# Optimization experiments

Hardware: AMD Instinct MI355X
Metric: run time of the kernel (lower is better)

## Reference

```python
import jax, jax.numpy as jnp
from jax import lax
import numpy as np

B = 32768      # batch
D = 256        # input = hidden = output dim
DEPTH = 9      # universal_depth


def setup_inputs() -> dict:
    key = jax.random.key(0)
    ks = jax.random.split(key, 16)
    s = 1.0 / np.sqrt(D)  # keep pre-activations sane
    r = lambda k, shp, sc=s: (jax.random.normal(k, shp, jnp.float32) * sc)
    return {
        "x": jax.random.normal(ks[0], (B, D), jnp.float32),
        "lin0_w": r(ks[1], (D, D)), "lin0_b": r(ks[2], (D,), 0.1),
        "lin1_w": r(ks[3], (D, D)), "lin1_b": r(ks[4], (D,), 0.1),
        "u1_w": jax.random.normal(ks[5], (DEPTH, D, D), jnp.float32),
        "u1_cw": r(ks[6], (D, D)), "u1_cb": r(ks[7], (D,), 0.1),
        "lin2_w": r(ks[8], (D, D)), "lin2_b": r(ks[9], (D,), 0.1),
        "u2_w": jax.random.normal(ks[10], (DEPTH, D, D), jnp.float32),
        "u2_cw": r(ks[11], (D, D)), "u2_cb": r(ks[12], (D,), 0.1),
        "lino_w": r(ks[13], (D, D)), "lino_b": r(ks[14], (D,), 0.1),
    }


def _universal_layer(x, uw, cw, cb):
    """UniversalNeuralLayer.forward, vectorized.

    The circulant 'gate' matrix implements, for state s of length n:
        s'[i] = cos*s[i] - sin*s[(i+1)%n] + sin*s[(i-1)%n]
    Applied 3 times per depth with angles uw[d, j, 0..2] (j = output unit).
    The result is independent of x and of the batch index.
    """
    n = x.shape[1]
    classical = x @ cw + cb                      # [B, n]
    # angle sequence per output j, in (depth, gate) order -> [3*DEPTH, n]
    angles = jnp.transpose(uw[:, :, :3], (0, 2, 1)).reshape(-1, n)
    init = jnp.full((n, n), 1.0 / np.sqrt(n), dtype=x.dtype)  # [n_j, n_state]

    def step(s, ang):
        c = jnp.cos(ang)[:, None]
        sn = jnp.sin(ang)[:, None]
        return c * s + sn * (jnp.roll(s, 1, axis=1) - jnp.roll(s, -1, axis=1)), None

    s, _ = lax.scan(step, init, angles)
    p = s[:, 0] ** 2                             # |state[0]|^2 per output j
    return jnp.tanh(classical + p[None, :])


def reference(x, lin0_w, lin0_b, lin1_w, lin1_b, u1_w, u1_cw, u1_cb,
              lin2_w, lin2_b, u2_w, u2_cw, u2_cb, lino_w, lino_b):
    h = jax.nn.relu(x @ lin0_w.T + lin0_b)
    h = jax.nn.relu(h @ lin1_w.T + lin1_b)
    h = _universal_layer(h, u1_w, u1_cw, u1_cb)
    h = jax.nn.relu(h @ lin2_w.T + lin2_b)
    h = _universal_layer(h, u2_w, u2_cw, u2_cb)
    return jax.nn.relu(h @ lino_w.T + lino_b)
```

## Files before the change

### kernel.cpp

```cpp
#include <hip/hip_runtime.h>
#include <math.h>

#define DD 256

typedef float  f32x4  __attribute__((ext_vector_type(4)));
typedef short  bf16x8 __attribute__((ext_vector_type(8)));

__device__ __forceinline__ unsigned short f2bf(float f) {
    unsigned int u = __float_as_uint(f);
    u = (u + 0x7fffu + ((u >> 16) & 1u)) >> 16;
    return (unsigned short)u;
}
__device__ __forceinline__ float bf2f(unsigned int h16) {
    return __uint_as_float(h16 << 16);
}

__global__ __launch_bounds__(256)
void universal_p_kernel(const float* __restrict__ u1_w,
                        const float* __restrict__ u2_w,
                        float* __restrict__ p_out ) {
    const int j = threadIdx.x;
    const float* uw = blockIdx.x ? u2_w : u1_w;
    float s = 0.0625f;
#pragma unroll
    for (int d = 0; d < 9; ++d)
#pragma unroll
        for (int g = 0; g < 3; ++g)
            s *= cosf(uw[d * DD * DD + j * DD + g]);
    p_out[blockIdx.x * DD + j] = s * s;
}

__global__ __launch_bounds__(256)
void prep_weights(const float* __restrict__ w0, const float* __restrict__ w1,
                  const float* __restrict__ cw1, const float* __restrict__ w2,
                  const float* __restrict__ cw2, const float* __restrict__ wo,
                  unsigned short* __restrict__ wall) {
    const int gid  = blockIdx.x * 256 + threadIdx.x;
    const int mat  = gid >> 13;
    const int rem  = gid & 8191;
    const int wb   = rem >> 11;
    const int rem2 = rem & 2047;
    const int k0   = rem2 >> 8;
    const int rem3 = rem2 & 255;
    const int nt   = rem3 >> 6;
    const int lane = rem3 & 63;
    const int n  = wb * 64 + nt * 16 + (lane & 15);
    const int kb = k0 * 32 + (lane >> 4) * 8;

    const float* src;
    bool tr = false;
    switch (mat) {
        case 0: src = w0; break;
        case 1: src = w1; break;
        case 2: src = cw1; tr = true; break;
        case 3: src = w2; break;
        case 4: src = cw2; tr = true; break;
        default: src = wo; break;
    }
    unsigned short tmp[8];
#pragma unroll
    for (int j = 0; j < 8; ++j) {
        const float v = tr ? src[(kb + j) * DD + n] : src[n * DD + kb + j];
        tmp[j] = f2bf(v);
    }
    *(uint4*)&wall[mat * 65536 + wb * 16384 + k0 * 2048 + nt * 512 + lane * 8] =
        *(const uint4*)tmp;
}

__device__ __forceinline__ int chunk_idx(int m, int kc) {
    return kc * 32 + (m ^ (kc & 7));
}

__device__ __forceinline__ float fast_tanh(float x) {
    const float e = __expf(2.0f * x);
    return 1.0f - 2.0f * __builtin_amdgcn_rcpf(1.0f + e);
}

template <int MODE>
__device__ __forceinline__ void layer_step(uint4* h, bf16x8 (&wr)[2][4],
                                           const unsigned short* __restrict__ W,
                                           const unsigned short* __restrict__ Wn,
                                           const float* __restrict__ bias,
                                           const float* __restrict__ pv) {
    const int tid  = threadIdx.x;
    const int wave = tid >> 6;
    const int lane = tid & 63;
    const int quad = lane >> 4;
    const int l15  = lane & 15;
    const unsigned short* Wb  = W  + wave * 16384 + lane * 8;
    const unsigned short* Wnb = Wn + wave * 16384 + lane * 8;

    f32x4 acc[4][2];
#pragma unroll
    for (int nt = 0; nt < 4; ++nt)
#pragma unroll
        for (int mt = 0; mt < 2; ++mt) acc[nt][mt] = (f32x4){0.f, 0.f, 0.f, 0.f};

    bf16x8 h_f[2][2];
#pragma unroll
    for (int mt = 0; mt < 2; ++mt)
        h_f[0][mt] = *(const bf16x8*)&h[chunk_idx(mt * 16 + l15, quad)];

#pragma unroll
    for (int k0 = 0; k0 < 8; ++k0) {
        const int cur = k0 & 1, nxt = cur ^ 1;
        {
            const unsigned short* ws = (k0 < 7) ? &Wb[(k0 + 1) * 2048] : Wnb;
#pragma unroll
            for (int nt = 0; nt < 4; ++nt)
                wr[nxt][nt] = *(const bf16x8*)&ws[nt * 512];
        }
        if (k0 < 7) {
            const int kc = (k0 + 1) * 4 + quad;
#pragma unroll
            for (int mt = 0; mt < 2; ++mt)
                h_f[nxt][mt] = *(const bf16x8*)&h[chunk_idx(mt * 16 + l15, kc)];
        }
#pragma unroll
        for (int nt = 0; nt < 4; ++nt)
#pragma unroll
            for (int mt = 0; mt < 2; ++mt)
                acc[nt][mt] = __builtin_amdgcn_mfma_f32_16x16x32_bf16(
                    wr[cur][nt], h_f[cur][mt], acc[nt][mt], 0, 0, 0);
    }

    __syncthreads();

    const int nb = wave * 64;
#pragma unroll
    for (int nt = 0; nt < 4; ++nt) {
        const int n0 = nb + nt * 16 + quad * 4;
        f32x4 add = *(const f32x4*)&bias[n0];
        if (MODE == 1) add += *(const f32x4*)&pv[n0];
        const int kc_o = n0 >> 3;
        const int half = quad & 1;
#pragma unroll
        for (int mt = 0; mt < 2; ++mt) {
            const f32x4 v = acc[nt][mt] + add;
            float t0, t1, t2, t3;
            if (MODE == 1) {
                t0 = fast_tanh(v.x); t1 = fast_tanh(v.y);
                t2 = fast_tanh(v.z); t3 = fast_tanh(v.w);
            } else {
                t0 = fmaxf(v.x, 0.f); t1 = fmaxf(v.y, 0.f);
                t2 = fmaxf(v.z, 0.f); t3 = fmaxf(v.w, 0.f);
            }
            uint2 u;
            u.x = (unsigned int)f2bf(t0) | ((unsigned int)f2bf(t1) << 16);
            u.y = (unsigned int)f2bf(t2) | ((unsigned int)f2bf(t3) << 16);
            *(uint2*)((char*)&h[chunk_idx(mt * 16 + l15, kc_o)] + half * 8) = u;
        }
    }
    __syncthreads();
}

__global__ __launch_bounds__(256, 2)
void unet_fused(const float* __restrict__ x,
                const unsigned short* __restrict__ wall,
                const float* __restrict__ b0, const float* __restrict__ b1,
                const float* __restrict__ cb1, const float* __restrict__ b2,
                const float* __restrict__ cb2, const float* __restrict__ bo,
                const float* __restrict__ pbuf,
                float* __restrict__ out) {
    __shared__ uint4 h[1024];
    const int m0 = blockIdx.x * 32;
    const int tid = threadIdx.x;
    const int wave = tid >> 6;
    const int lane = tid & 63;

    bf16x8 wr[2][4];
    {
        const unsigned short* ws = wall + wave * 16384 + lane * 8;
#pragma unroll
        for (int nt = 0; nt < 4; ++nt)
            wr[0][nt] = *(const bf16x8*)&ws[nt * 512];
    }

    const int c4 = tid & 63;
    const int rbase = (tid >> 6) * 8;
    const int kc_s = c4 >> 1;
    const int half_s = c4 & 1;
#pragma unroll
    for (int i = 0; i < 8; ++i) {
        const int row = rbase + i;
        const float4 v = *(const float4*)&x[(size_t)(m0 + row) * DD + c4 * 4];
        uint2 u;
        u.x = (unsigned int)f2bf(v.x) | ((unsigned int)f2bf(v.y) << 16);
        u.y = (unsigned int)f2bf(v.z) | ((unsigned int)f2bf(v.w) << 16);
        *(uint2*)((char*)&h[chunk_idx(row, kc_s)] + half_s * 8) = u;
    }
    __syncthreads();

    layer_step<0>(h, wr, wall + 0 * 65536, wall + 1 * 65536, b0, nullptr);
    layer_step<0>(h, wr, wall + 1 * 65536, wall + 2 * 65536, b1, nullptr);
    layer_step<1>(h, wr, wall + 2 * 65536, wall + 3 * 65536, cb1, pbuf);
    layer_step<0>(h, wr, wall + 3 * 65536, wall + 4 * 65536, b2, nullptr);
    layer_step<1>(h, wr, wall + 4 * 65536, wall + 5 * 65536, cb2, pbuf + 256);
    layer_step<0>(h, wr, wall + 5 * 65536, wall + 0 * 65536, bo, nullptr);

#pragma unroll
    for (int i = 0; i < 8; ++i) {
        const int row = rbase + i;
        const uint2 u = *(const uint2*)((char*)&h[chunk_idx(row, kc_s)] + half_s * 8);
        float4 v;
        v.x = bf2f(u.x & 0xffffu); v.y = bf2f(u.x >> 16);
        v.z = bf2f(u.y & 0xffffu); v.w = bf2f(u.y >> 16);
        *(float4*)&out[(size_t)(m0 + row) * DD + c4 * 4] = v;
    }
}

extern "C" void kernel_launch(void* const* d_in, const int* in_sizes, int n_in,
                              void* d_out, int out_size, void* d_ws, size_t ws_size,
                              hipStream_t stream) {
    const float* x      = (const float*)d_in[0];
    const float* lin0_w = (const float*)d_in[1];
    const float* lin0_b = (const float*)d_in[2];
    const float* lin1_w = (const float*)d_in[3];
    const float* lin1_b = (const float*)d_in[4];
    const float* u1_w   = (const float*)d_in[5];
    const float* u1_cw  = (const float*)d_in[6];
    const float* u1_cb  = (const float*)d_in[7];
    const float* lin2_w = (const float*)d_in[8];
    const float* lin2_b = (const float*)d_in[9];
    const float* u2_w   = (const float*)d_in[10];
    const float* u2_cw  = (const float*)d_in[11];
    const float* u2_cb  = (const float*)d_in[12];
    const float* lino_w = (const float*)d_in[13];
    const float* lino_b = (const float*)d_in[14];

    float* out = (float*)d_out;
    unsigned short* wall = (unsigned short*)d_ws;
    float* pbuf = (float*)((char*)d_ws + 6 * 65536 * 2);

    universal_p_kernel<<<dim3(2), dim3(256), 0, stream>>>(u1_w, u2_w, pbuf);
    prep_weights<<<dim3(192), dim3(256), 0, stream>>>(
        lin0_w, lin1_w, u1_cw, lin2_w, u2_cw, lino_w, wall);
    unet_fused<<<dim3(1024), dim3(256), 0, stream>>>(
        x, wall, lin0_b, lin1_b, u1_cb, lin2_b, u2_cb, lino_b, pbuf, out);
}
```

Before: 154.8 us.

## Double-buffer LDS activations, merge prep kernels, write final layer directly to global

Activations now ping-pong between two LDS buffers, so each layer needs only one barrier instead of two, using a lighter waitcnt-plus-barrier. The last layer writes fp32 ReLU results straight from the accumulators to global memory, which removes the bf16 round trip through LDS and also keeps the output in full precision. The two setup kernels are merged into one launch, and the occupancy hint rises to 4 blocks per CU. The cost is doubled LDS per block (32KB) and possible register pressure under the tighter launch bound.

```diff
diff --git a/kernel.cpp b/kernel.cpp
--- a/kernel.cpp
+++ b/kernel.cpp
@@ -16,25 +16,24 @@
 }
 
 __global__ __launch_bounds__(256)
-void universal_p_kernel(const float* __restrict__ u1_w,
-                        const float* __restrict__ u2_w,
-                        float* __restrict__ p_out ) {
-    const int j = threadIdx.x;
-    const float* uw = blockIdx.x ? u2_w : u1_w;
-    float s = 0.0625f;
-#pragma unroll
-    for (int d = 0; d < 9; ++d)
-#pragma unroll
-        for (int g = 0; g < 3; ++g)
-            s *= cosf(uw[d * DD * DD + j * DD + g]);
-    p_out[blockIdx.x * DD + j] = s * s;
-}
-
-__global__ __launch_bounds__(256)
-void prep_weights(const float* __restrict__ w0, const float* __restrict__ w1,
-                  const float* __restrict__ cw1, const float* __restrict__ w2,
-                  const float* __restrict__ cw2, const float* __restrict__ wo,
-                  unsigned short* __restrict__ wall) {
+void prep_all(const float* __restrict__ w0, const float* __restrict__ w1,
+              const float* __restrict__ cw1, const float* __restrict__ w2,
+              const float* __restrict__ cw2, const float* __restrict__ wo,
+              const float* __restrict__ u1_w, const float* __restrict__ u2_w,
+              unsigned short* __restrict__ wall, float* __restrict__ p_out) {
+    if (blockIdx.x >= 192) {
+        const int j = threadIdx.x;
+        const int which = blockIdx.x - 192;
+        const float* uw = which ? u2_w : u1_w;
+        float s = 0.0625f;
+#pragma unroll
+        for (int d = 0; d < 9; ++d)
+#pragma unroll
+            for (int g = 0; g < 3; ++g)
+                s *= cosf(uw[d * DD * DD + j * DD + g]);
+        p_out[which * DD + j] = s * s;
+        return;
+    }
     const int gid  = blockIdx.x * 256 + threadIdx.x;
     const int mat  = gid >> 13;
     const int rem  = gid & 8191;
@@ -76,19 +75,24 @@
     return 1.0f - 2.0f * __builtin_amdgcn_rcpf(1.0f + e);
 }
 
+__device__ __forceinline__ void lds_barrier() {
+    asm volatile("s_waitcnt lgkmcnt(0)" ::: "memory");
+    __builtin_amdgcn_s_barrier();
+}
+
 template <int MODE>
-__device__ __forceinline__ void layer_step(uint4* h, bf16x8 (&wr)[2][4],
-                                           const unsigned short* __restrict__ W,
-                                           const unsigned short* __restrict__ Wn,
+__device__ __forceinline__ void layer_step(const uint4* hr, uint4* hw,
+                                           bf16x8 (&wr)[2][4],
+                                           const unsigned short* __restrict__ Wb,
+                                           const unsigned short* __restrict__ Wnb,
                                            const float* __restrict__ bias,
-                                           const float* __restrict__ pv) {
+                                           const float* __restrict__ pv,
+                                           float* __restrict__ out, int m0) {
     const int tid  = threadIdx.x;
     const int wave = tid >> 6;
     const int lane = tid & 63;
     const int quad = lane >> 4;
     const int l15  = lane & 15;
-    const unsigned short* Wb  = W  + wave * 16384 + lane * 8;
-    const unsigned short* Wnb = Wn + wave * 16384 + lane * 8;
 
     f32x4 acc[4][2];
 #pragma unroll
@@ -99,7 +103,7 @@
     bf16x8 h_f[2][2];
 #pragma unroll
     for (int mt = 0; mt < 2; ++mt)
-        h_f[0][mt] = *(const bf16x8*)&h[chunk_idx(mt * 16 + l15, quad)];
+        h_f[0][mt] = *(const bf16x8*)&hr[chunk_idx(mt * 16 + l15, quad)];
 
 #pragma unroll
     for (int k0 = 0; k0 < 8; ++k0) {
@@ -114,7 +118,7 @@
             const int kc = (k0 + 1) * 4 + quad;
 #pragma unroll
             for (int mt = 0; mt < 2; ++mt)
-                h_f[nxt][mt] = *(const bf16x8*)&h[chunk_idx(mt * 16 + l15, kc)];
+                h_f[nxt][mt] = *(const bf16x8*)&hr[chunk_idx(mt * 16 + l15, kc)];
         }
 #pragma unroll
         for (int nt = 0; nt < 4; ++nt)
@@ -124,37 +128,48 @@
                     wr[cur][nt], h_f[cur][mt], acc[nt][mt], 0, 0, 0);
     }
 
-    __syncthreads();
-
     const int nb = wave * 64;
+    f32x4 addv[4];
 #pragma unroll
     for (int nt = 0; nt < 4; ++nt) {
         const int n0 = nb + nt * 16 + quad * 4;
-        f32x4 add = *(const f32x4*)&bias[n0];
-        if (MODE == 1) add += *(const f32x4*)&pv[n0];
+        addv[nt] = *(const f32x4*)&bias[n0];
+        if (MODE == 1) addv[nt] += *(const f32x4*)&pv[n0];
+    }
+
+#pragma unroll
+    for (int nt = 0; nt < 4; ++nt) {
+        const int n0   = nb + nt * 16 + quad * 4;
         const int kc_o = n0 >> 3;
         const int half = quad & 1;
 #pragma unroll
         for (int mt = 0; mt < 2; ++mt) {
-            const f32x4 v = acc[nt][mt] + add;
-            float t0, t1, t2, t3;
-            if (MODE == 1) {
-                t0 = fast_tanh(v.x); t1 = fast_tanh(v.y);
-                t2 = fast_tanh(v.z); t3 = fast_tanh(v.w);
+            const f32x4 v = acc[nt][mt] + addv[nt];
+            if (MODE == 2) {
+                f32x4 r;
+                r.x = fmaxf(v.x, 0.f); r.y = fmaxf(v.y, 0.f);
+                r.z = fmaxf(v.z, 0.f); r.w = fmaxf(v.w, 0.f);
+                *(f32x4*)&out[(size_t)(m0 + mt * 16 + l15) * DD + n0] = r;
             } else {
-                t0 = fmaxf(v.x, 0.f); t1 = fmaxf(v.y, 0.f);
-                t2 = fmaxf(v.z, 0.f); t3 = fmaxf(v.w, 0.f);
+                float t0, t1, t2, t3;
+                if (MODE == 1) {
+                    t0 = fast_tanh(v.x); t1 = fast_tanh(v.y);
+                    t2 = fast_tanh(v.z); t3 = fast_tanh(v.w);
+                } else {
+                    t0 = fmaxf(v.x, 0.f); t1 = fmaxf(v.y, 0.f);
+                    t2 = fmaxf(v.z, 0.f); t3 = fmaxf(v.w, 0.f);
+                }
+                uint2 u;
+                u.x = (unsigned int)f2bf(t0) | ((unsigned int)f2bf(t1) << 16);
+                u.y = (unsigned int)f2bf(t2) | ((unsigned int)f2bf(t3) << 16);
+                *(uint2*)((char*)&hw[chunk_idx(mt * 16 + l15, kc_o)] + half * 8) = u;
             }
-            uint2 u;
-            u.x = (unsigned int)f2bf(t0) | ((unsigned int)f2bf(t1) << 16);
-            u.y = (unsigned int)f2bf(t2) | ((unsigned int)f2bf(t3) << 16);
-            *(uint2*)((char*)&h[chunk_idx(mt * 16 + l15, kc_o)] + half * 8) = u;
         }
     }
-    __syncthreads();
-}
-
-__global__ __launch_bounds__(256, 2)
+    if (MODE != 2) lds_barrier();
+}
+
+__global__ __launch_bounds__(256, 4)
 void unet_fused(const float* __restrict__ x,
                 const unsigned short* __restrict__ wall,
                 const float* __restrict__ b0, const float* __restrict__ b1,
@@ -162,23 +177,24 @@
                 const float* __restrict__ cb2, const float* __restrict__ bo,
                 const float* __restrict__ pbuf,
                 float* __restrict__ out) {
-    __shared__ uint4 h[1024];
-    const int m0 = blockIdx.x * 32;
-    const int tid = threadIdx.x;
+    __shared__ uint4 hbuf[2048];
+    uint4* hA = hbuf;
+    uint4* hB = hbuf + 1024;
+    const int m0   = blockIdx.x * 32;
+    const int tid  = threadIdx.x;
     const int wave = tid >> 6;
     const int lane = tid & 63;
 
+    const unsigned short* WB = wall + wave * 16384 + lane * 8;
+
     bf16x8 wr[2][4];
-    {
-        const unsigned short* ws = wall + wave * 16384 + lane * 8;
-#pragma unroll
-        for (int nt = 0; nt < 4; ++nt)
-            wr[0][nt] = *(const bf16x8*)&ws[nt * 512];
-    }
-
-    const int c4 = tid & 63;
-    const int rbase = (tid >> 6) * 8;
-    const int kc_s = c4 >> 1;
+#pragma unroll
+    for (int nt = 0; nt < 4; ++nt)
+        wr[0][nt] = *(const bf16x8*)&WB[nt * 512];
+
+    const int c4     = tid & 63;
+    const int rbase  = wave * 8;
+    const int kc_s   = c4 >> 1;
     const int half_s = c4 & 1;
 #pragma unroll
     for (int i = 0; i < 8; ++i) {
@@ -187,26 +203,22 @@
         uint2 u;
         u.x = (unsigned int)f2bf(v.x) | ((unsigned int)f2bf(v.y) << 16);
         u.y = (unsigned int)f2bf(v.z) | ((unsigned int)f2bf(v.w) << 16);
-        *(uint2*)((char*)&h[chunk_idx(row, kc_s)] + half_s * 8) = u;
-    }
-    __syncthreads();
-
-    layer_step<0>(h, wr, wall + 0 * 65536, wall + 1 * 65536, b0, nullptr);
-    layer_step<0>(h, wr, wall + 1 * 65536, wall + 2 * 65536, b1, nullptr);
-    layer_step<1>(h, wr, wall + 2 * 65536, wall + 3 * 65536, cb1, pbuf);
-    layer_step<0>(h, wr, wall + 3 * 65536, wall + 4 * 65536, b2, nullptr);
-    layer_step<1>(h, wr, wall + 4 * 65536, wall + 5 * 65536, cb2, pbuf + 256);
-    layer_step<0>(h, wr, wall + 5 * 65536, wall + 0 * 65536, bo, nullptr);
-
-#pragma unroll
-    for (int i = 0; i < 8; ++i) {
-        const int row = rbase + i;
-        const uint2 u = *(const uint2*)((char*)&h[chunk_idx(row, kc_s)] + half_s * 8);
-        float4 v;
-        v.x = bf2f(u.x & 0xffffu); v.y = bf2f(u.x >> 16);
-        v.z = bf2f(u.y & 0xffffu); v.w = bf2f(u.y >> 16);
-        *(float4*)&out[(size_t)(m0 + row) * DD + c4 * 4] = v;
-    }
+        *(uint2*)((char*)&hA[chunk_idx(row, kc_s)] + half_s * 8) = u;
+    }
+    lds_barrier();
+
+    layer_step<0>(hA, hB, wr, WB + 0 * 65536, WB + 1 * 65536, b0, nullptr,
+                  nullptr, 0);
+    layer_step<0>(hB, hA, wr, WB + 1 * 65536, WB + 2 * 65536, b1, nullptr,
+                  nullptr, 0);
+    layer_step<1>(hA, hB, wr, WB + 2 * 65536, WB + 3 * 65536, cb1, pbuf,
+                  nullptr, 0);
+    layer_step<0>(hB, hA, wr, WB + 3 * 65536, WB + 4 * 65536, b2, nullptr,
+                  nullptr, 0);
+    layer_step<1>(hA, hB, wr, WB + 4 * 65536, WB + 5 * 65536, cb2, pbuf + 256,
+                  nullptr, 0);
+    layer_step<2>(hB, nullptr, wr, WB + 5 * 65536, WB + 0 * 65536, bo, nullptr,
+                  out, m0);
 }
 
 extern "C" void kernel_launch(void* const* d_in, const int* in_sizes, int n_in,
@@ -232,9 +244,8 @@
     unsigned short* wall = (unsigned short*)d_ws;
     float* pbuf = (float*)((char*)d_ws + 6 * 65536 * 2);
 
-    universal_p_kernel<<<dim3(2), dim3(256), 0, stream>>>(u1_w, u2_w, pbuf);
-    prep_weights<<<dim3(192), dim3(256), 0, stream>>>(
-        lin0_w, lin1_w, u1_cw, lin2_w, u2_cw, lino_w, wall);
+    prep_all<<<dim3(194), dim3(256), 0, stream>>>(
+        lin0_w, lin1_w, u1_cw, lin2_w, u2_cw, lino_w, u1_w, u2_w, wall, pbuf);
     unet_fused<<<dim3(1024), dim3(256), 0, stream>>>(
         x, wall, lin0_b, lin1_b, u1_cb, lin2_b, u2_cb, lino_b, pbuf, out);
 }
```

Result: slower. 158.0 us (+2.1%).
